# Optimization experiments

Measured on AMD Instinct MI355X. Metric: run time of the kernel, lower is better.

The kernel has to match this reference:

```python
import jax, jax.numpy as jnp
import numpy as np

HEADS1, HID = 2, 128
OUT_FEATS = 256
K, M = 8, 128


def _gat_conv(x, src, dst, W, a_src, a_dst, bias, heads, out_dim, concat, neg_slope):
    """PyG-style GATConv: linear -> per-edge leakyrelu attention -> dst-softmax -> scatter-sum."""
    N = x.shape[0]
    h = (x @ W.T).reshape(N, heads, out_dim)          # [N, H, D]
    alpha_src = jnp.sum(h * a_src, axis=-1)            # [N, H]
    alpha_dst = jnp.sum(h * a_dst, axis=-1)            # [N, H]
    e = jax.nn.leaky_relu(alpha_src[src] + alpha_dst[dst], neg_slope)  # [E, H]
    # numerically stable segment softmax over incoming edges per destination
    m = jax.ops.segment_max(e, dst, num_segments=N)    # [N, H]
    e = jnp.exp(e - m[dst])
    s = jax.ops.segment_sum(e, dst, num_segments=N)    # [N, H]
    alpha = e / s[dst]                                  # [E, H]
    msg = h[src] * alpha[:, :, None]                    # [E, H, D]
    out = jax.ops.segment_sum(msg, dst, num_segments=N)  # [N, H, D]
    out = out.reshape(N, heads * out_dim) if concat else out.mean(axis=1)
    return out + bias


def setup_inputs() -> dict:
    key = jax.random.key(0)
    ks = jax.random.split(key, 14)
    N, E, IN = 50000, 800000, 256
    x = jax.random.normal(ks[0], (N, IN), dtype=jnp.float32)
    edge_index = jax.random.randint(ks[1], (2, E), 0, N, dtype=jnp.int64)
    sc = 0.1
    return {
        "x": x,
        "edge_index": edge_index,
        "W1": jax.random.normal(ks[2], (HEADS1 * HID, IN), dtype=jnp.float32) * sc,
        "a_src1": jax.random.normal(ks[3], (HEADS1, HID), dtype=jnp.float32) * sc,
        "a_dst1": jax.random.normal(ks[4], (HEADS1, HID), dtype=jnp.float32) * sc,
        "b1": jax.random.normal(ks[5], (HEADS1 * HID,), dtype=jnp.float32) * sc,
        "W2": jax.random.normal(ks[6], (OUT_FEATS, HEADS1 * HID), dtype=jnp.float32) * sc,
        "a_src2": jax.random.normal(ks[7], (1, OUT_FEATS), dtype=jnp.float32) * sc,
        "a_dst2": jax.random.normal(ks[8], (1, OUT_FEATS), dtype=jnp.float32) * sc,
        "b2": jax.random.normal(ks[9], (OUT_FEATS,), dtype=jnp.float32) * sc,
        "g": jax.random.normal(ks[10], (OUT_FEATS, K * M), dtype=jnp.float32) * sc,
        "mu": jax.random.normal(ks[11], (K, M), dtype=jnp.float32) * sc,
    }


def reference(x, edge_index, W1, a_src1, a_dst1, b1, W2, a_src2, a_dst2, b2, g, mu):
    N = x.shape[0]
    loops = jnp.arange(N, dtype=edge_index.dtype)  # PyG GATConv adds self-loops by default
    src = jnp.concatenate([edge_index[0], loops])
    dst = jnp.concatenate([edge_index[1], loops])
    h = _gat_conv(x, src, dst, W1, a_src1, a_dst1, b1, HEADS1, HID, True, 0.2)
    h = jax.nn.leaky_relu(h, 0.01)  # F.leaky_relu default slope
    h = _gat_conv(h, src, dst, W2, a_src2, a_dst2, b2, 1, OUT_FEATS, False, 0.2)
    out = (h @ g).reshape(N, K, M)                      # [N, K, M]
    # cosine similarity against mu along M (torch eps=1e-8)
    num = jnp.einsum('nkm,km->nk', out, mu)
    denom = jnp.maximum(
        jnp.linalg.norm(out, axis=-1) * jnp.linalg.norm(mu, axis=-1)[None, :], 1e-8
    )
    return num / denom  # [N, K]
```

## Files before the change

### kernel.cpp

```cpp
#include <hip/hip_runtime.h>
#include <math.h>

typedef short s16x8 __attribute__((ext_vector_type(8)));
typedef float f32x4 __attribute__((ext_vector_type(4)));

__device__ __forceinline__ float lrelu(float x, float s) { return x > 0.0f ? x : s * x; }

__device__ __forceinline__ unsigned short f2bf(float f) {
  unsigned int u = __float_as_uint(f);
  u = (u + 0x7FFFu + ((u >> 16) & 1u)) >> 16;
  return (unsigned short)u;
}
__device__ __forceinline__ float bf2f(unsigned short h) {
  return __uint_as_float(((unsigned int)h) << 16);
}
__device__ __forceinline__ float bcastf(float v, int l) {
  return __uint_as_float((unsigned)__builtin_amdgcn_readlane((int)__float_as_uint(v), l));
}

__device__ __forceinline__ void gload_lds16(void* lds, const void* g) {
  __builtin_amdgcn_global_load_lds(
      (const __attribute__((address_space(1))) unsigned int*)g,
      (__attribute__((address_space(3))) unsigned int*)lds, 16, 0, 0);
}

__global__ void deg_kernel(const int* __restrict__ dst, int* __restrict__ deg, int E) {
  int e = blockIdx.x * blockDim.x + threadIdx.x;
  if (e < E) atomicAdd(&deg[dst[e]], 1);
}

__global__ __launch_bounds__(256) void bsum_kernel(const int* __restrict__ deg,
                                                   int* __restrict__ bsum, int N) {
  int t = blockIdx.x * 256 + threadIdx.x;
  int v = (t < N) ? deg[t] : 0;
  #pragma unroll
  for (int off = 1; off < 64; off <<= 1) v += __shfl_xor(v, off, 64);
  __shared__ int ws[4];
  if ((threadIdx.x & 63) == 0) ws[threadIdx.x >> 6] = v;
  __syncthreads();
  if (threadIdx.x == 0) bsum[blockIdx.x] = ws[0] + ws[1] + ws[2] + ws[3];
}

__global__ __launch_bounds__(256) void bscan_kernel(const int* __restrict__ bsum,
                                                    int* __restrict__ boff, int nb,
                                                    int* __restrict__ rowptr_total) {
  __shared__ int s[256];
  int t = threadIdx.x;
  int v = (t < nb) ? bsum[t] : 0;
  s[t] = v;
  __syncthreads();
  for (int off = 1; off < 256; off <<= 1) {
    int u = (t >= off) ? s[t - off] : 0;
    __syncthreads();
    s[t] += u;
    __syncthreads();
  }
  if (t < nb) boff[t] = s[t] - v;
  if (t == nb - 1) *rowptr_total = s[t];
}

__global__ __launch_bounds__(256) void bwrite_kernel(const int* __restrict__ deg,
                                                     const int* __restrict__ boff,
                                                     int* __restrict__ rowptr,
                                                     int* __restrict__ cursor, int N) {
  __shared__ int s[256];
  int t = blockIdx.x * 256 + threadIdx.x;
  int v = (t < N) ? deg[t] : 0;
  s[threadIdx.x] = v;
  __syncthreads();
  for (int off = 1; off < 256; off <<= 1) {
    int u = (threadIdx.x >= off) ? s[threadIdx.x - off] : 0;
    __syncthreads();
    s[threadIdx.x] += u;
    __syncthreads();
  }
  if (t < N) {
    int ex = boff[blockIdx.x] + s[threadIdx.x] - v;
    rowptr[t] = ex;
    cursor[t] = ex;
  }
}

__global__ void fill_kernel(const int* __restrict__ src, const int* __restrict__ dst,
                            int* __restrict__ cursor, int* __restrict__ colsrc, int E) {
  int e = blockIdx.x * blockDim.x + threadIdx.x;
  if (e < E) {
    int d = dst[e];
    int pos = atomicAdd(&cursor[d], 1);
    colsrc[pos] = src[e];
  }
}

__global__ void cvt_rows_kernel(const float* __restrict__ src, unsigned short* __restrict__ dst,
                                int nrows, int prows) {
  int t = blockIdx.x * blockDim.x + threadIdx.x;
  int row = t >> 6;
  int c = (t & 63) * 4;
  if (row >= prows) return;
  float4 v = make_float4(0.f, 0.f, 0.f, 0.f);
  if (row < nrows) v = *(const float4*)&src[(size_t)row * 256 + c];
  ushort4 o;
  o.x = f2bf(v.x); o.y = f2bf(v.y); o.z = f2bf(v.z); o.w = f2bf(v.w);
  *(ushort4*)&dst[(size_t)row * 256 + c] = o;
}

__global__ void cvt_gT_kernel(const float* __restrict__ g, unsigned short* __restrict__ gT) {
  int idx = blockIdx.x * blockDim.x + threadIdx.x;
  int k = idx >> 10, n = idx & 1023;
  gT[(size_t)n * 256 + k] = f2bf(g[idx]);
}

template<int EPI, int AH>
__global__ __launch_bounds__(256, 2) void gemm_bf16(
    const unsigned short* __restrict__ A, const unsigned short* __restrict__ B,
    unsigned short* __restrict__ Cb,
    const float* __restrict__ avs, const float* __restrict__ avd,
    float* __restrict__ asrcO, float* __restrict__ adstO,
    const float* __restrict__ mu, const float* __restrict__ nmu,
    float* __restrict__ outcos, int M)
{
  __shared__ unsigned short As[128 * 64];
  __shared__ unsigned short Bs[128 * 64];
  const int t = threadIdx.x;
  const int w = t >> 6;
  const int l = t & 63;
  const int m0 = blockIdx.x * 128;
  const int n0 = blockIdx.y * 128;

  f32x4 acc[2][8];
  #pragma unroll
  for (int i = 0; i < 2; ++i)
    #pragma unroll
    for (int j = 0; j < 8; ++j) acc[i][j] = (f32x4){0.f, 0.f, 0.f, 0.f};

  const unsigned char* Ab = (const unsigned char*)A;
  const unsigned char* Bb = (const unsigned char*)B;
  unsigned char* AsB = (unsigned char*)As;
  unsigned char* BsB = (unsigned char*)Bs;

  const int srow = l >> 3;
  const int gchk = (l & 7) ^ srow;

  for (int kb = 0; kb < 256; kb += 64) {
    #pragma unroll
    for (int i = 0; i < 4; ++i) {
      int seg = w * 4 + i;
      int row = seg * 8 + srow;
      gload_lds16(AsB + seg * 1024,
                  Ab + (size_t)(m0 + row) * 512 + kb * 2 + gchk * 16);
      gload_lds16(BsB + seg * 1024,
                  Bb + (size_t)(n0 + row) * 512 + kb * 2 + gchk * 16);
    }
    asm volatile("s_waitcnt vmcnt(0)" ::: "memory");
    __syncthreads();

    const int rl = l & 15;
    const int kc = l >> 4;
    #pragma unroll
    for (int ks = 0; ks < 2; ++ks) {
      s16x8 af[2], bfr[8];
      #pragma unroll
      for (int mf = 0; mf < 2; ++mf) {
        int r = w * 32 + mf * 16 + rl;
        int slot = (ks * 4 + kc) ^ (r & 7);
        af[mf] = *(const s16x8*)&As[r * 64 + slot * 8];
      }
      #pragma unroll
      for (int nf = 0; nf < 8; ++nf) {
        int r = nf * 16 + rl;
        int slot = (ks * 4 + kc) ^ (r & 7);
        bfr[nf] = *(const s16x8*)&Bs[r * 64 + slot * 8];
      }
      #pragma unroll
      for (int mf = 0; mf < 2; ++mf)
        #pragma unroll
        for (int nf = 0; nf < 8; ++nf)
          acc[mf][nf] = __builtin_amdgcn_mfma_f32_16x16x32_bf16(af[mf], bfr[nf], acc[mf][nf], 0, 0, 0);
    }
    __syncthreads();
  }

  if (EPI == 0) {
    #pragma unroll
    for (int mf = 0; mf < 2; ++mf)
      #pragma unroll
      for (int nf = 0; nf < 8; ++nf)
        #pragma unroll
        for (int j = 0; j < 4; ++j) {
          int r = m0 + w * 32 + mf * 16 + (l >> 4) * 4 + j;
          int c = n0 + nf * 16 + (l & 15);
          Cb[(size_t)r * 256 + c] = f2bf(acc[mf][nf][j]);
        }
    if (AH > 0) {
      float avS[8], avD[8];
      #pragma unroll
      for (int nf = 0; nf < 8; ++nf) {
        avS[nf] = avs[n0 + nf * 16 + (l & 15)];
        avD[nf] = avd[n0 + nf * 16 + (l & 15)];
      }
      #pragma unroll
      for (int mf = 0; mf < 2; ++mf)
        #pragma unroll
        for (int j = 0; j < 4; ++j) {
          float ds = 0.f, dd = 0.f;
          #pragma unroll
          for (int nf = 0; nf < 8; ++nf) {
            float o = acc[mf][nf][j];
            ds = fmaf(o, avS[nf], ds);
            dd = fmaf(o, avD[nf], dd);
          }
          #pragma unroll
          for (int off = 1; off < 16; off <<= 1) {
            ds += __shfl_xor(ds, off, 64);
            dd += __shfl_xor(dd, off, 64);
          }
          if ((l & 15) == 0) {
            int r = m0 + w * 32 + mf * 16 + (l >> 4) * 4 + j;
            if (r < M) {
              if (AH == 2) {
                asrcO[(size_t)r * 2 + blockIdx.y] = ds;
                adstO[(size_t)r * 2 + blockIdx.y] = dd;
              } else {
                atomicAdd(&asrcO[r], ds);
                atomicAdd(&adstO[r], dd);
              }
            }
          }
        }
    }
  } else {
    const int kchunk = blockIdx.y;
    float nm = nmu[kchunk];
    float mv[8];
    #pragma unroll
    for (int nf = 0; nf < 8; ++nf) mv[nf] = mu[kchunk * 128 + nf * 16 + (l & 15)];
    #pragma unroll
    for (int mf = 0; mf < 2; ++mf)
      #pragma unroll
      for (int j = 0; j < 4; ++j) {
        float num = 0.f, ss = 0.f;
        #pragma unroll
        for (int nf = 0; nf < 8; ++nf) {
          float o = acc[mf][nf][j];
          num = fmaf(o, mv[nf], num);
          ss  = fmaf(o, o, ss);
        }
        #pragma unroll
        for (int off = 1; off < 16; off <<= 1) {
          num += __shfl_xor(num, off, 64);
          ss  += __shfl_xor(ss, off, 64);
        }
        if ((l & 15) == 0) {
          int r = m0 + w * 32 + mf * 16 + (l >> 4) * 4 + j;
          if (r < M) outcos[(size_t)r * 8 + kchunk] = num / fmaxf(sqrtf(ss) * nm, 1e-8f);
        }
      }
  }
}

template<int H, bool OUT_LRELU>
__global__ __launch_bounds__(256) void agg_kernel(
    const unsigned short* __restrict__ hin, const float* __restrict__ asrc,
    const float* __restrict__ adst, const int* __restrict__ rowptr,
    const int* __restrict__ colsrc, const float* __restrict__ bias,
    unsigned short* __restrict__ outp, int N)
{
  int wid  = threadIdx.x >> 6;
  int lane = threadIdx.x & 63;
  int n = blockIdx.x * 4 + wid;
  if (n >= N) return;
  const int head = (H == 2) ? (lane >> 5) : 0;

  int beg = rowptr[n], end = rowptr[n + 1];

  float ad0 = adst[(size_t)n * H + 0];
  float ad1 = (H == 2) ? adst[(size_t)n * 2 + 1] : 0.f;
  float m0 = lrelu(asrc[(size_t)n * H + 0] + ad0, 0.2f);
  float m1 = (H == 2) ? lrelu(asrc[(size_t)n * 2 + 1] + ad1, 0.2f) : 0.f;
  float s0 = 1.f, s1 = 1.f;

  float acc[4];
  {
    ushort4 hv = *(const ushort4*)&hin[(size_t)n * 256 + lane * 4];
    acc[0] = bf2f(hv.x); acc[1] = bf2f(hv.y);
    acc[2] = bf2f(hv.z); acc[3] = bf2f(hv.w);
  }

  for (int cbeg = beg; cbeg < end; cbeg += 64) {
    int cnt = end - cbeg; if (cnt > 64) cnt = 64;
    int src_i = 0;
    float e0 = -1e30f, e1 = -1e30f;
    if (lane < cnt) {
      src_i = colsrc[cbeg + lane];
      if (H == 2) {
        float2 av = *(const float2*)&asrc[(size_t)src_i * 2];
        e0 = lrelu(av.x + ad0, 0.2f);
        e1 = lrelu(av.y + ad1, 0.2f);
      } else {
        e0 = lrelu(asrc[src_i] + ad0, 0.2f);
      }
    }
    float c0 = e0, c1 = e1;
    #pragma unroll
    for (int off = 32; off >= 1; off >>= 1) {
      c0 = fmaxf(c0, __shfl_xor(c0, off, 64));
      if (H == 2) c1 = fmaxf(c1, __shfl_xor(c1, off, 64));
    }
    float nm0 = fmaxf(m0, c0);
    float r0 = __expf(m0 - nm0); m0 = nm0;
    float r1 = 1.f;
    if (H == 2) { float nm1 = fmaxf(m1, c1); r1 = __expf(m1 - nm1); m1 = nm1; }
    s0 *= r0; if (H == 2) s1 *= r1;
    float rh = (H == 2 && head) ? r1 : r0;
    #pragma unroll
    for (int k = 0; k < 4; ++k) acc[k] *= rh;
    float p0 = (lane < cnt) ? __expf(e0 - m0) : 0.f;
    float p1 = (H == 2 && lane < cnt) ? __expf(e1 - m1) : 0.f;
    float t0 = p0, t1 = p1;
    #pragma unroll
    for (int off = 32; off >= 1; off >>= 1) {
      t0 += __shfl_xor(t0, off, 64);
      if (H == 2) t1 += __shfl_xor(t1, off, 64);
    }
    s0 += t0; if (H == 2) s1 += t1;

    int ne4 = (cnt + 3) & ~3;
    for (int e = 0; e < ne4; e += 4) {
      ushort4 v[4]; float aw[4];
      #pragma unroll
      for (int u = 0; u < 4; ++u) {
        int sidx = __builtin_amdgcn_readlane(src_i, e + u);
        float a0 = bcastf(p0, e + u);
        if (H == 2) {
          float a1 = bcastf(p1, e + u);
          aw[u] = head ? a1 : a0;
        } else {
          aw[u] = a0;
        }
        v[u] = *(const ushort4*)&hin[(size_t)sidx * 256 + lane * 4];
      }
      #pragma unroll
      for (int u = 0; u < 4; ++u) {
        acc[0] = fmaf(bf2f(v[u].x), aw[u], acc[0]);
        acc[1] = fmaf(bf2f(v[u].y), aw[u], acc[1]);
        acc[2] = fmaf(bf2f(v[u].z), aw[u], acc[2]);
        acc[3] = fmaf(bf2f(v[u].w), aw[u], acc[3]);
      }
    }
  }

  float sh = (H == 2 && head) ? s1 : s0;
  float inv = 1.0f / sh;
  float4 bv = *(const float4*)&bias[lane * 4];
  float o0 = acc[0] * inv + bv.x, o1 = acc[1] * inv + bv.y;
  float o2 = acc[2] * inv + bv.z, o3 = acc[3] * inv + bv.w;
  if (OUT_LRELU) {
    o0 = lrelu(o0, 0.01f); o1 = lrelu(o1, 0.01f);
    o2 = lrelu(o2, 0.01f); o3 = lrelu(o3, 0.01f);
  }
  ushort4 o;
  o.x = f2bf(o0); o.y = f2bf(o1); o.z = f2bf(o2); o.w = f2bf(o3);
  *(ushort4*)&outp[(size_t)n * 256 + lane * 4] = o;
}

__global__ __launch_bounds__(64) void munorm_kernel(const float* __restrict__ mu,
                                                    float* __restrict__ norm_mu) {
  int lane = threadIdx.x;
  for (int k = 0; k < 8; ++k) {
    float v0 = mu[k * 128 + lane];
    float v1 = mu[k * 128 + 64 + lane];
    float s = v0 * v0 + v1 * v1;
    #pragma unroll
    for (int off = 1; off < 64; off <<= 1) s += __shfl_xor(s, off, 64);
    if (lane == 0) norm_mu[k] = sqrtf(s);
  }
}

extern "C" void kernel_launch(void* const* d_in, const int* in_sizes, int n_in,
                              void* d_out, int out_size, void* d_ws, size_t ws_size,
                              hipStream_t stream) {
  const float* x      = (const float*)d_in[0];
  const int*   ei     = (const int*)  d_in[1];
  const float* W1     = (const float*)d_in[2];
  const float* a_src1 = (const float*)d_in[3];
  const float* a_dst1 = (const float*)d_in[4];
  const float* b1     = (const float*)d_in[5];
  const float* W2     = (const float*)d_in[6];
  const float* a_src2 = (const float*)d_in[7];
  const float* a_dst2 = (const float*)d_in[8];
  const float* b2     = (const float*)d_in[9];
  const float* g      = (const float*)d_in[10];
  const float* mu     = (const float*)d_in[11];

  const int N  = in_sizes[0] / 256;
  const int E  = in_sizes[1] / 2;
  const int Mp = ((N + 127) / 128) * 128;
  const int nb = (N + 255) / 256;
  const int* src = ei;
  const int* dst = ei + E;

  unsigned short* us = (unsigned short*)d_ws;
  size_t off = 0;
  unsigned short* xb  = us + off; off += (size_t)Mp * 256;
  unsigned short* h1b = us + off; off += (size_t)Mp * 256;
  unsigned short* o1b = us + off; off += (size_t)Mp * 256;
  unsigned short* h2b = us + off; off += (size_t)Mp * 256;
  unsigned short* o2b = xb;
  float* f = (float*)(us + off);
  size_t fo = 0;
  float* asrc1 = f + fo; fo += (size_t)N * 2;
  float* adst1 = f + fo; fo += (size_t)N * 2;
  float* asrc2 = f + fo; fo += N;
  float* adst2 = f + fo; fo += N;
  float* nmu   = f + fo; fo += 8;
  int* deg    = (int*)(f + fo);
  int* rowptr = deg + N;
  int* cursor = rowptr + N + 1;
  int* colsrc = cursor + N;
  int* bsum   = colsrc + E;
  int* boff   = bsum + 256;
  unsigned short* w1b = (unsigned short*)(boff + 256);
  unsigned short* w2b = w1b + 256 * 256;
  unsigned short* gTb = w2b + 256 * 256;

  hipMemsetAsync(deg, 0, (size_t)N * sizeof(int), stream);
  hipMemsetAsync(asrc2, 0, (size_t)N * 2 * sizeof(float), stream);
  deg_kernel<<<(E + 255) / 256, 256, 0, stream>>>(dst, deg, E);
  bsum_kernel<<<nb, 256, 0, stream>>>(deg, bsum, N);
  bscan_kernel<<<1, 256, 0, stream>>>(bsum, boff, nb, rowptr + N);
  bwrite_kernel<<<nb, 256, 0, stream>>>(deg, boff, rowptr, cursor, N);
  fill_kernel<<<(E + 255) / 256, 256, 0, stream>>>(src, dst, cursor, colsrc, E);

  cvt_rows_kernel<<<Mp / 4, 256, 0, stream>>>(x, xb, N, Mp);
  cvt_rows_kernel<<<64, 256, 0, stream>>>(W1, w1b, 256, 256);
  cvt_rows_kernel<<<64, 256, 0, stream>>>(W2, w2b, 256, 256);
  cvt_gT_kernel<<<1024, 256, 0, stream>>>(g, gTb);
  munorm_kernel<<<1, 64, 0, stream>>>(mu, nmu);

  const int gm = Mp / 128;

  gemm_bf16<0, 2><<<dim3(gm, 2), 256, 0, stream>>>(xb, w1b, h1b,
      a_src1, a_dst1, asrc1, adst1, nullptr, nullptr, nullptr, N);
  agg_kernel<2, true><<<(N + 3) / 4, 256, 0, stream>>>(h1b, asrc1, adst1, rowptr, colsrc, b1, o1b, N);

  gemm_bf16<0, 1><<<dim3(gm, 2), 256, 0, stream>>>(o1b, w2b, h2b,
      a_src2, a_dst2, asrc2, adst2, nullptr, nullptr, nullptr, N);
  agg_kernel<1, false><<<(N + 3) / 4, 256, 0, stream>>>(h2b, asrc2, adst2, rowptr, colsrc, b2, o2b, N);

  gemm_bf16<1, 0><<<dim3(gm, 8), 256, 0, stream>>>(o2b, gTb, nullptr,
      nullptr, nullptr, nullptr, nullptr, mu, nmu, (float*)d_out, N);
}
```

Baseline: 416.7 us.

## Keep A tile in registers across N tiles, merge weight setup, widen agg unroll

The GEMM now loads each block's 128-row A panel into registers once and loops over all N tiles inside the block. B tiles are double-buffered in LDS with the next load prefetched during the current MFMAs, which removes the repeated A reloads and the separate y-dimension blocks. The small weight-conversion and mu-norm kernels are merged into one launch to cut launch overhead. The aggregation gather loop is unrolled from 4 to 8 edges to get more loads in flight. In exchange, each GEMM launch has fewer blocks, the held A fragments raise register pressure, and the wider unroll does more padded work on low-degree nodes.

```diff
diff --git a/kernel.cpp b/kernel.cpp
--- a/kernel.cpp
+++ b/kernel.cpp
@@ -104,13 +104,43 @@
   *(ushort4*)&dst[(size_t)row * 256 + c] = o;
 }
 
-__global__ void cvt_gT_kernel(const float* __restrict__ g, unsigned short* __restrict__ gT) {
-  int idx = blockIdx.x * blockDim.x + threadIdx.x;
-  int k = idx >> 10, n = idx & 1023;
-  gT[(size_t)n * 256 + k] = f2bf(g[idx]);
-}
-
-template<int EPI, int AH>
+__global__ __launch_bounds__(256) void wsetup_kernel(
+    const float* __restrict__ W1, const float* __restrict__ W2,
+    const float* __restrict__ g, const float* __restrict__ mu,
+    unsigned short* __restrict__ w1b, unsigned short* __restrict__ w2b,
+    unsigned short* __restrict__ gTb, float* __restrict__ nmu) {
+  int b = blockIdx.x;
+  int t = threadIdx.x;
+  if (b < 128) {
+    const float* S = (b < 64) ? W1 : W2;
+    unsigned short* D = (b < 64) ? w1b : w2b;
+    int bb = b & 63;
+    int row = bb * 4 + (t >> 6);
+    int c = (t & 63) * 4;
+    float4 v = *(const float4*)&S[(size_t)row * 256 + c];
+    ushort4 o;
+    o.x = f2bf(v.x); o.y = f2bf(v.y); o.z = f2bf(v.z); o.w = f2bf(v.w);
+    *(ushort4*)&D[(size_t)row * 256 + c] = o;
+  } else if (b < 1152) {
+    int idx = (b - 128) * 256 + t;
+    int k = idx >> 10, n = idx & 1023;
+    gTb[(size_t)n * 256 + k] = f2bf(g[idx]);
+  } else {
+    if (t < 64) {
+      int lane = t;
+      for (int k = 0; k < 8; ++k) {
+        float v0 = mu[k * 128 + lane];
+        float v1 = mu[k * 128 + 64 + lane];
+        float s = v0 * v0 + v1 * v1;
+        #pragma unroll
+        for (int off = 1; off < 64; off <<= 1) s += __shfl_xor(s, off, 64);
+        if (lane == 0) nmu[k] = sqrtf(s);
+      }
+    }
+  }
+}
+
+template<int EPI, int AH, int NT>
 __global__ __launch_bounds__(256, 2) void gemm_bf16(
     const unsigned short* __restrict__ A, const unsigned short* __restrict__ B,
     unsigned short* __restrict__ Cb,
@@ -119,142 +149,170 @@
     const float* __restrict__ mu, const float* __restrict__ nmu,
     float* __restrict__ outcos, int M)
 {
-  __shared__ unsigned short As[128 * 64];
-  __shared__ unsigned short Bs[128 * 64];
+  __shared__ unsigned short Bs[2][128 * 64];
   const int t = threadIdx.x;
   const int w = t >> 6;
   const int l = t & 63;
   const int m0 = blockIdx.x * 128;
-  const int n0 = blockIdx.y * 128;
-
-  f32x4 acc[2][8];
-  #pragma unroll
-  for (int i = 0; i < 2; ++i)
-    #pragma unroll
-    for (int j = 0; j < 8; ++j) acc[i][j] = (f32x4){0.f, 0.f, 0.f, 0.f};
+  const int rl = l & 15;
+  const int kc = l >> 4;
+  const int srow = l >> 3;
+  const int gchk = (l & 7) ^ srow;
 
   const unsigned char* Ab = (const unsigned char*)A;
   const unsigned char* Bb = (const unsigned char*)B;
-  unsigned char* AsB = (unsigned char*)As;
-  unsigned char* BsB = (unsigned char*)Bs;
-
-  const int srow = l >> 3;
-  const int gchk = (l & 7) ^ srow;
-
-  for (int kb = 0; kb < 256; kb += 64) {
+
+  s16x8 af[4][2][2];
+  #pragma unroll
+  for (int kb = 0; kb < 4; ++kb) {
+    unsigned char* buf = (unsigned char*)&Bs[kb & 1][0];
     #pragma unroll
     for (int i = 0; i < 4; ++i) {
       int seg = w * 4 + i;
       int row = seg * 8 + srow;
-      gload_lds16(AsB + seg * 1024,
-                  Ab + (size_t)(m0 + row) * 512 + kb * 2 + gchk * 16);
-      gload_lds16(BsB + seg * 1024,
-                  Bb + (size_t)(n0 + row) * 512 + kb * 2 + gchk * 16);
-    }
-    asm volatile("s_waitcnt vmcnt(0)" ::: "memory");
-    __syncthreads();
-
-    const int rl = l & 15;
-    const int kc = l >> 4;
-    #pragma unroll
-    for (int ks = 0; ks < 2; ++ks) {
-      s16x8 af[2], bfr[8];
+      gload_lds16(buf + seg * 1024,
+                  Ab + (size_t)(m0 + row) * 512 + kb * 128 + gchk * 16);
+    }
+    __syncthreads();
+    #pragma unroll
+    for (int ks = 0; ks < 2; ++ks)
       #pragma unroll
       for (int mf = 0; mf < 2; ++mf) {
         int r = w * 32 + mf * 16 + rl;
         int slot = (ks * 4 + kc) ^ (r & 7);
-        af[mf] = *(const s16x8*)&As[r * 64 + slot * 8];
-      }
-      #pragma unroll
-      for (int nf = 0; nf < 8; ++nf) {
-        int r = nf * 16 + rl;
-        int slot = (ks * 4 + kc) ^ (r & 7);
-        bfr[nf] = *(const s16x8*)&Bs[r * 64 + slot * 8];
-      }
+        af[kb][ks][mf] = *(const s16x8*)&Bs[kb & 1][r * 64 + slot * 8];
+      }
+    __syncthreads();
+  }
+
+  {
+    unsigned char* buf = (unsigned char*)&Bs[0][0];
+    #pragma unroll
+    for (int i = 0; i < 4; ++i) {
+      int seg = w * 4 + i;
+      int row = seg * 8 + srow;
+      gload_lds16(buf + seg * 1024,
+                  Bb + (size_t)row * 512 + gchk * 16);
+    }
+  }
+  __syncthreads();
+
+  for (int nt = 0; nt < NT; ++nt) {
+    f32x4 acc[2][8];
+    #pragma unroll
+    for (int i = 0; i < 2; ++i)
+      #pragma unroll
+      for (int j = 0; j < 8; ++j) acc[i][j] = (f32x4){0.f, 0.f, 0.f, 0.f};
+
+    #pragma unroll
+    for (int kb = 0; kb < 4; ++kb) {
+      bool last = (nt == NT - 1) && (kb == 3);
+      if (!last) {
+        int nnt = nt + (kb == 3);
+        int nkb = (kb + 1) & 3;
+        unsigned char* buf = (unsigned char*)&Bs[(kb + 1) & 1][0];
+        #pragma unroll
+        for (int i = 0; i < 4; ++i) {
+          int seg = w * 4 + i;
+          int row = seg * 8 + srow;
+          gload_lds16(buf + seg * 1024,
+                      Bb + (size_t)(nnt * 128 + row) * 512 + nkb * 128 + gchk * 16);
+        }
+      }
+      #pragma unroll
+      for (int ks = 0; ks < 2; ++ks) {
+        s16x8 bfr[8];
+        #pragma unroll
+        for (int nf = 0; nf < 8; ++nf) {
+          int r = nf * 16 + rl;
+          int slot = (ks * 4 + kc) ^ (r & 7);
+          bfr[nf] = *(const s16x8*)&Bs[kb & 1][r * 64 + slot * 8];
+        }
+        #pragma unroll
+        for (int mf = 0; mf < 2; ++mf)
+          #pragma unroll
+          for (int nf = 0; nf < 8; ++nf)
+            acc[mf][nf] = __builtin_amdgcn_mfma_f32_16x16x32_bf16(af[kb][ks][mf], bfr[nf], acc[mf][nf], 0, 0, 0);
+      }
+      __syncthreads();
+    }
+
+    if (EPI == 0) {
+      int n0 = nt * 128;
       #pragma unroll
       for (int mf = 0; mf < 2; ++mf)
         #pragma unroll
         for (int nf = 0; nf < 8; ++nf)
-          acc[mf][nf] = __builtin_amdgcn_mfma_f32_16x16x32_bf16(af[mf], bfr[nf], acc[mf][nf], 0, 0, 0);
-    }
-    __syncthreads();
-  }
-
-  if (EPI == 0) {
-    #pragma unroll
-    for (int mf = 0; mf < 2; ++mf)
-      #pragma unroll
-      for (int nf = 0; nf < 8; ++nf)
+          #pragma unroll
+          for (int j = 0; j < 4; ++j) {
+            int r = m0 + w * 32 + mf * 16 + (l >> 4) * 4 + j;
+            int c = n0 + nf * 16 + rl;
+            Cb[(size_t)r * 256 + c] = f2bf(acc[mf][nf][j]);
+          }
+      if (AH > 0) {
+        float avS[8], avD[8];
+        #pragma unroll
+        for (int nf = 0; nf < 8; ++nf) {
+          avS[nf] = avs[n0 + nf * 16 + rl];
+          avD[nf] = avd[n0 + nf * 16 + rl];
+        }
+        #pragma unroll
+        for (int mf = 0; mf < 2; ++mf)
+          #pragma unroll
+          for (int j = 0; j < 4; ++j) {
+            float ds = 0.f, dd = 0.f;
+            #pragma unroll
+            for (int nf = 0; nf < 8; ++nf) {
+              float o = acc[mf][nf][j];
+              ds = fmaf(o, avS[nf], ds);
+              dd = fmaf(o, avD[nf], dd);
+            }
+            #pragma unroll
+            for (int off = 1; off < 16; off <<= 1) {
+              ds += __shfl_xor(ds, off, 64);
+              dd += __shfl_xor(dd, off, 64);
+            }
+            if (rl == 0) {
+              int r = m0 + w * 32 + mf * 16 + (l >> 4) * 4 + j;
+              if (r < M) {
+                if (AH == 2) {
+                  asrcO[(size_t)r * 2 + nt] = ds;
+                  adstO[(size_t)r * 2 + nt] = dd;
+                } else {
+                  atomicAdd(&asrcO[r], ds);
+                  atomicAdd(&adstO[r], dd);
+                }
+              }
+            }
+          }
+      }
+    } else {
+      float nm = nmu[nt];
+      float mv[8];
+      #pragma unroll
+      for (int nf = 0; nf < 8; ++nf) mv[nf] = mu[nt * 128 + nf * 16 + rl];
+      #pragma unroll
+      for (int mf = 0; mf < 2; ++mf)
         #pragma unroll
         for (int j = 0; j < 4; ++j) {
-          int r = m0 + w * 32 + mf * 16 + (l >> 4) * 4 + j;
-          int c = n0 + nf * 16 + (l & 15);
-          Cb[(size_t)r * 256 + c] = f2bf(acc[mf][nf][j]);
-        }
-    if (AH > 0) {
-      float avS[8], avD[8];
-      #pragma unroll
-      for (int nf = 0; nf < 8; ++nf) {
-        avS[nf] = avs[n0 + nf * 16 + (l & 15)];
-        avD[nf] = avd[n0 + nf * 16 + (l & 15)];
-      }
-      #pragma unroll
-      for (int mf = 0; mf < 2; ++mf)
-        #pragma unroll
-        for (int j = 0; j < 4; ++j) {
-          float ds = 0.f, dd = 0.f;
+          float num = 0.f, ss = 0.f;
           #pragma unroll
           for (int nf = 0; nf < 8; ++nf) {
             float o = acc[mf][nf][j];
-            ds = fmaf(o, avS[nf], ds);
-            dd = fmaf(o, avD[nf], dd);
+            num = fmaf(o, mv[nf], num);
+            ss  = fmaf(o, o, ss);
           }
           #pragma unroll
           for (int off = 1; off < 16; off <<= 1) {
-            ds += __shfl_xor(ds, off, 64);
-            dd += __shfl_xor(dd, off, 64);
+            num += __shfl_xor(num, off, 64);
+            ss  += __shfl_xor(ss, off, 64);
           }
-          if ((l & 15) == 0) {
+          if (rl == 0) {
             int r = m0 + w * 32 + mf * 16 + (l >> 4) * 4 + j;
-            if (r < M) {
-              if (AH == 2) {
-                asrcO[(size_t)r * 2 + blockIdx.y] = ds;
-                adstO[(size_t)r * 2 + blockIdx.y] = dd;
-              } else {
-                atomicAdd(&asrcO[r], ds);
-                atomicAdd(&adstO[r], dd);
-              }
-            }
+            if (r < M) outcos[(size_t)r * 8 + nt] = num / fmaxf(sqrtf(ss) * nm, 1e-8f);
           }
         }
     }
-  } else {
-    const int kchunk = blockIdx.y;
-    float nm = nmu[kchunk];
-    float mv[8];
-    #pragma unroll
-    for (int nf = 0; nf < 8; ++nf) mv[nf] = mu[kchunk * 128 + nf * 16 + (l & 15)];
-    #pragma unroll
-    for (int mf = 0; mf < 2; ++mf)
-      #pragma unroll
-      for (int j = 0; j < 4; ++j) {
-        float num = 0.f, ss = 0.f;
-        #pragma unroll
-        for (int nf = 0; nf < 8; ++nf) {
-          float o = acc[mf][nf][j];
-          num = fmaf(o, mv[nf], num);
-          ss  = fmaf(o, o, ss);
-        }
-        #pragma unroll
-        for (int off = 1; off < 16; off <<= 1) {
-          num += __shfl_xor(num, off, 64);
-          ss  += __shfl_xor(ss, off, 64);
-        }
-        if ((l & 15) == 0) {
-          int r = m0 + w * 32 + mf * 16 + (l >> 4) * 4 + j;
-          if (r < M) outcos[(size_t)r * 8 + kchunk] = num / fmaxf(sqrtf(ss) * nm, 1e-8f);
-        }
-      }
   }
 }
 
@@ -324,11 +382,11 @@
     }
     s0 += t0; if (H == 2) s1 += t1;
 
-    int ne4 = (cnt + 3) & ~3;
-    for (int e = 0; e < ne4; e += 4) {
-      ushort4 v[4]; float aw[4];
-      #pragma unroll
-      for (int u = 0; u < 4; ++u) {
+    int ne8 = (cnt + 7) & ~7;
+    for (int e = 0; e < ne8; e += 8) {
+      ushort4 v[8]; float aw[8];
+      #pragma unroll
+      for (int u = 0; u < 8; ++u) {
         int sidx = __builtin_amdgcn_readlane(src_i, e + u);
         float a0 = bcastf(p0, e + u);
         if (H == 2) {
@@ -340,7 +398,7 @@
         v[u] = *(const ushort4*)&hin[(size_t)sidx * 256 + lane * 4];
       }
       #pragma unroll
-      for (int u = 0; u < 4; ++u) {
+      for (int u = 0; u < 8; ++u) {
         acc[0] = fmaf(bf2f(v[u].x), aw[u], acc[0]);
         acc[1] = fmaf(bf2f(v[u].y), aw[u], acc[1]);
         acc[2] = fmaf(bf2f(v[u].z), aw[u], acc[2]);
@@ -361,19 +419,6 @@
   ushort4 o;
   o.x = f2bf(o0); o.y = f2bf(o1); o.z = f2bf(o2); o.w = f2bf(o3);
   *(ushort4*)&outp[(size_t)n * 256 + lane * 4] = o;
-}
-
-__global__ __launch_bounds__(64) void munorm_kernel(const float* __restrict__ mu,
-                                                    float* __restrict__ norm_mu) {
-  int lane = threadIdx.x;
-  for (int k = 0; k < 8; ++k) {
-    float v0 = mu[k * 128 + lane];
-    float v1 = mu[k * 128 + 64 + lane];
-    float s = v0 * v0 + v1 * v1;
-    #pragma unroll
-    for (int off = 1; off < 64; off <<= 1) s += __shfl_xor(s, off, 64);
-    if (lane == 0) norm_mu[k] = sqrtf(s);
-  }
 }
 
 extern "C" void kernel_launch(void* const* d_in, const int* in_sizes, int n_in,
@@ -432,21 +477,18 @@
   fill_kernel<<<(E + 255) / 256, 256, 0, stream>>>(src, dst, cursor, colsrc, E);
 
   cvt_rows_kernel<<<Mp / 4, 256, 0, stream>>>(x, xb, N, Mp);
-  cvt_rows_kernel<<<64, 256, 0, stream>>>(W1, w1b, 256, 256);
-  cvt_rows_kernel<<<64, 256, 0, stream>>>(W2, w2b, 256, 256);
-  cvt_gT_kernel<<<1024, 256, 0, stream>>>(g, gTb);
-  munorm_kernel<<<1, 64, 0, stream>>>(mu, nmu);
+  wsetup_kernel<<<1153, 256, 0, stream>>>(W1, W2, g, mu, w1b, w2b, gTb, nmu);
 
   const int gm = Mp / 128;
 
-  gemm_bf16<0, 2><<<dim3(gm, 2), 256, 0, stream>>>(xb, w1b, h1b,
+  gemm_bf16<0, 2, 2><<<gm, 256, 0, stream>>>(xb, w1b, h1b,
       a_src1, a_dst1, asrc1, adst1, nullptr, nullptr, nullptr, N);
   agg_kernel<2, true><<<(N + 3) / 4, 256, 0, stream>>>(h1b, asrc1, adst1, rowptr, colsrc, b1, o1b, N);
 
-  gemm_bf16<0, 1><<<dim3(gm, 2), 256, 0, stream>>>(o1b, w2b, h2b,
+  gemm_bf16<0, 1, 2><<<gm, 256, 0, stream>>>(o1b, w2b, h2b,
       a_src2, a_dst2, asrc2, adst2, nullptr, nullptr, nullptr, N);
   agg_kernel<1, false><<<(N + 3) / 4, 256, 0, stream>>>(h2b, asrc2, adst2, rowptr, colsrc, b2, o2b, N);
 
-  gemm_bf16<1, 0><<<dim3(gm, 8), 256, 0, stream>>>(o2b, gTb, nullptr,
+  gemm_bf16<1, 0, 8><<<gm, 256, 0, stream>>>(o2b, gTb, nullptr,
       nullptr, nullptr, nullptr, nullptr, mu, nmu, (float*)d_out, N);
 }
```

Result: no change. 417.7 us (+0.2%).
